# Optimization experiments

Measured on AMD Instinct MI355X. Metric: run time of the kernel, lower is better.

Reference implementation:

```python
import jax, jax.numpy as jnp
import numpy as np

B, N, D = 8, 2048, 768
K, H, G = 256, 12, 4
DH = D // H          # 64
EPS = 1e-12


def grouped_pointwise(x, w):
    """Grouped Conv1d with kernel_size=1, no bias.
    x: (b, n, d); w: (g, out_per_g, in_per_g) [torch weight (d, d/g, 1) reshaped].
    """
    b, n, d = x.shape
    g = w.shape[0]
    xg = x.reshape(b, n, g, d // g)
    return jnp.einsum('bngi,goi->bngo', xg, w).reshape(b, n, d)


def setup_inputs() -> dict:
    key = jax.random.key(0)
    ks = jax.random.split(key, 8)
    std_conv = 1.0 / np.sqrt(D // G)   # torch conv default ~ U(-sqrt(1/fan_in), ...)
    std_pk = 1.0 / np.sqrt(K)          # init_ uses last dim of (seq_len, k_dim)
    std_lin = 1.0 / np.sqrt(D)
    return {
        'input_embedding': jax.random.normal(ks[0], (B, N, D), jnp.float32),
        'wq': jax.random.uniform(ks[1], (G, D // G, D // G), jnp.float32, -std_conv, std_conv),
        'wk': jax.random.uniform(ks[2], (G, D // G, D // G), jnp.float32, -std_conv, std_conv),
        'project_k': jax.random.uniform(ks[3], (N, K), jnp.float32, -std_pk, std_pk),
        'w_out': jax.random.uniform(ks[4], (D, D), jnp.float32, -std_lin, std_lin),
        'b_out': jax.random.uniform(ks[5], (D,), jnp.float32, -std_lin, std_lin),
        'gamma': jnp.ones((D,), jnp.float32),
        'beta': jnp.zeros((D,), jnp.float32),
    }


def reference(input_embedding, wq, wk, project_k, w_out, b_out, gamma, beta):
    x = input_embedding                       # (b, n, d)
    b, n, d = x.shape

    queries = grouped_pointwise(x, wq)        # (b, n, d)
    k_raw = grouped_pointwise(x, wk)          # (b, n, d)  (key conv)
    k_proj = jnp.einsum('bnd,nk->bkd', k_raw, project_k)   # (b, K, d)

    # Faithful replication of: keys.permute(0,2,1).view(b, K, h, dh)
    # (memory-reinterpreting reshape of the (b, d, K) layout)
    keys = jnp.transpose(k_proj, (0, 2, 1)).reshape(b, K, H, DH)
    keys = jnp.transpose(keys, (0, 2, 1, 3))                # (b, h, K, dh)

    # values also come from the key conv (self.value unused in source forward)
    values = k_proj.reshape(b, K, H, DH).transpose(0, 2, 1, 3)   # (b, h, K, dh)
    q = queries.reshape(b, n, H, DH).transpose(0, 2, 1, 3)       # (b, h, n, dh)

    dots = jnp.einsum('bhnd,bhkd->bhnk', q, keys) / np.sqrt(DH)
    attn = jax.nn.softmax(dots, axis=-1)      # dropout = identity (eval)
    ctx = jnp.einsum('bhnk,bhkd->bhnd', attn, values)
    ctx = ctx.transpose(0, 2, 1, 3).reshape(b, n, d)

    out = ctx @ w_out.T + b_out               # nn.Linear
    y = x + out                               # residual
    mu = jnp.mean(y, axis=-1, keepdims=True)
    var = jnp.mean((y - mu) ** 2, axis=-1, keepdims=True)
    return (y - mu) / jnp.sqrt(var + EPS) * gamma + beta
```

## Files before the change

### kernel.cpp

```cpp
#include <hip/hip_runtime.h>
#include <hip/hip_bf16.h>

typedef short short8 __attribute__((ext_vector_type(8)));
typedef short short4v __attribute__((ext_vector_type(4)));
typedef int i32x4 __attribute__((ext_vector_type(4)));
typedef float f32x4 __attribute__((ext_vector_type(4)));

#define MFMA(a, b, c) __builtin_amdgcn_mfma_f32_16x16x32_bf16((a), (b), (c), 0, 0, 0)

__device__ __forceinline__ short f2bf(float f) {
  unsigned u = __builtin_bit_cast(unsigned, f);
  unsigned r = u + 0x7FFFu + ((u >> 16) & 1u);
  return (short)(r >> 16);
}

__device__ __forceinline__ float bf2f(short s) {
  unsigned u = ((unsigned)(unsigned short)s) << 16;
  return __builtin_bit_cast(float, u);
}

__device__ __forceinline__ short8 cvt8(float4 a, float4 b) {
  short8 t;
  t[0] = f2bf(a.x); t[1] = f2bf(a.y); t[2] = f2bf(a.z); t[3] = f2bf(a.w);
  t[4] = f2bf(b.x); t[5] = f2bf(b.y); t[6] = f2bf(b.z); t[7] = f2bf(b.w);
  return t;
}

__global__ __launch_bounds__(256) void k_prep_xt(
    const float* __restrict__ wq, const float* __restrict__ wk,
    const float* __restrict__ wout, const float* __restrict__ pk,
    short* __restrict__ wqb, short* __restrict__ wkb,
    short* __restrict__ woutb, short* __restrict__ pkT,
    const float* __restrict__ x, short* __restrict__ xbT)
{
  __shared__ short Ls[64][78];
  const int bid = blockIdx.x, tid = threadIdx.x;
  if (bid < 2304) {
    int idx = bid * 256 + tid;
    if (idx < 147456) { wqb[idx] = f2bf(wq[idx]); wkb[idx] = f2bf(wk[idx]); }
    if (idx < 589824) { woutb[idx] = f2bf(wout[idx]); }
    if (idx < 524288) {
      int n = idx >> 8, k = idx & 255;
      pkT[(size_t)k * 2048 + n] = f2bf(pk[idx]);
    }
    return;
  }
  const int bid2 = bid - 2304;
  const int e0 = (bid2 % 12) * 64;
  const int n0 = ((bid2 / 12) % 32) * 64;
  const int b  = bid2 / 384;
  const int r = tid >> 2, ci = (tid & 3) * 16;
  const float* src = x + ((size_t)b * 2048 + n0 + r) * 768 + e0 + ci;
#pragma unroll
  for (int ii = 0; ii < 4; ii++) {
    float4 v = *(const float4*)(src + ii * 4);
    short4v s; s[0] = f2bf(v.x); s[1] = f2bf(v.y); s[2] = f2bf(v.z); s[3] = f2bf(v.w);
    *(short4v*)&Ls[r][ci + ii * 4] = s;
  }
  __syncthreads();
  const int ep = tid >> 2, no = (tid & 3) * 16;
  short8 o0, o1;
#pragma unroll
  for (int u = 0; u < 8; u++) o0[u] = Ls[no + u][ep];
#pragma unroll
  for (int u = 0; u < 8; u++) o1[u] = Ls[no + 8 + u][ep];
  short* dst = xbT + ((size_t)b * 768 + e0 + ep) * 2048 + n0 + no;
  *(short8*)dst = o0;
  *(short8*)(dst + 8) = o1;
}

__global__ __launch_bounds__(256, 2) void k_conv(
    const float* __restrict__ x, const short* __restrict__ wqb,
    short* __restrict__ qo)
{
  __shared__ __align__(16) short Xs[64][40];
  const int tid = threadIdx.x, lane = tid & 63, w = tid >> 6;
  const int g = blockIdx.y;
  const int m0 = blockIdx.x * 64;
  const int wr = (w >> 1) * 32, wcol = (w & 1) * 96;
  const int lrow = lane & 15, lk8 = (lane >> 4) * 8;

  f32x4 acc[2][6];
#pragma unroll
  for (int mi = 0; mi < 2; mi++)
#pragma unroll
    for (int cf = 0; cf < 6; cf++) acc[mi][cf] = (f32x4)0.f;

  const int xr = tid >> 2;
  const int xc = (tid & 3) * 8;
  const float* xsrc = x + (size_t)(m0 + xr) * 768 + g * 192 + xc;

  for (int k0 = 0; k0 < 192; k0 += 32) {
    __syncthreads();
    {
      float4 v0 = *(const float4*)(xsrc + k0);
      float4 v1 = *(const float4*)(xsrc + k0 + 4);
      *(short8*)&Xs[xr][xc] = cvt8(v0, v1);
    }
    __syncthreads();
    short8 a0 = *(const short8*)&Xs[wr + lrow][lk8];
    short8 a1 = *(const short8*)&Xs[wr + 16 + lrow][lk8];
#pragma unroll
    for (int cf = 0; cf < 6; cf++) {
      short8 bb = *(const short8*)(wqb + ((size_t)g * 192 + wcol + cf * 16 + lrow) * 192 + k0 + lk8);
      acc[0][cf] = MFMA(a0, bb, acc[0][cf]);
      acc[1][cf] = MFMA(a1, bb, acc[1][cf]);
    }
  }
#pragma unroll
  for (int mi = 0; mi < 2; mi++)
#pragma unroll
    for (int cf = 0; cf < 6; cf++)
#pragma unroll
      for (int j = 0; j < 4; j++) {
        int m = m0 + wr + mi * 16 + (lane >> 4) * 4 + j;
        qo[(size_t)m * 768 + g * 192 + wcol + cf * 16 + lrow] = f2bf(acc[mi][cf][j]);
      }
}

__global__ __launch_bounds__(512, 4) void k_xproj(
    const short* __restrict__ pkT, const short* __restrict__ xbT,
    float* __restrict__ xproj)
{
  __shared__ __align__(16) short A2[2][64][72];
  __shared__ __align__(16) short B2[2][64][72];
  const int tid = threadIdx.x, lane = tid & 63, w = tid >> 6;
  const int f = blockIdx.x;
  const int xcd = f & 7, rem = f >> 3;
  const int k2t4 = rem & 3, eb8 = rem >> 2;
  const int e_b = eb8 * 8 + xcd;
  const int k2t = k2t4 * 64;
  const int et = (e_b % 12) * 64, b = e_b / 12;
  const int lrow = lane & 15, g4 = lane >> 4, lk8 = g4 * 8;
  const int wa = (w & 3) * 16, wb = (w >> 2) * 32;

  const int r = tid >> 3, c8 = tid & 7;
  const short* aSrc = pkT + (size_t)(k2t + r) * 2048 + c8 * 8;
  const short* bSrc = xbT + ((size_t)b * 768 + et + r) * 2048 + c8 * 8;

  {
    short8 gA = *(const short8*)aSrc;
    short8 gB = *(const short8*)bSrc;
    *(short8*)&A2[0][r][c8 * 8] = gA;
    *(short8*)&B2[0][r][c8 * 8] = gB;
  }
  __syncthreads();

  f32x4 acc[2];
  acc[0] = (f32x4)0.f; acc[1] = (f32x4)0.f;

  short8 gA, gB;
#pragma unroll 2
  for (int t = 0; t < 32; ++t) {
    const int cur = t & 1;
    if (t < 31) {
      gA = *(const short8*)(aSrc + (t + 1) * 64);
      gB = *(const short8*)(bSrc + (t + 1) * 64);
    }
    short8 af0 = *(const short8*)&A2[cur][wa + lrow][lk8];
    short8 af1 = *(const short8*)&A2[cur][wa + lrow][32 + lk8];
    short8 bf00 = *(const short8*)&B2[cur][wb + lrow][lk8];
    short8 bf01 = *(const short8*)&B2[cur][wb + lrow][32 + lk8];
    short8 bf10 = *(const short8*)&B2[cur][wb + 16 + lrow][lk8];
    short8 bf11 = *(const short8*)&B2[cur][wb + 16 + lrow][32 + lk8];
    acc[0] = MFMA(af0, bf00, acc[0]);
    acc[0] = MFMA(af1, bf01, acc[0]);
    acc[1] = MFMA(af0, bf10, acc[1]);
    acc[1] = MFMA(af1, bf11, acc[1]);
    if (t < 31) {
      *(short8*)&A2[cur ^ 1][r][c8 * 8] = gA;
      *(short8*)&B2[cur ^ 1][r][c8 * 8] = gB;
    }
    __syncthreads();
  }

  float* dst = xproj + ((size_t)b * 256 + k2t + wa) * 768 + et + wb;
#pragma unroll
  for (int cf = 0; cf < 2; cf++)
#pragma unroll
    for (int j = 0; j < 4; j++)
      dst[(size_t)(g4 * 4 + j) * 768 + cf * 16 + lrow] = acc[cf][j];
}

__global__ __launch_bounds__(256) void k_kconv(
    float* xpio, const short* __restrict__ wkb)
{
  const int tid = threadIdx.x, lane = tid & 63, w = tid >> 6;
  const int rt = blockIdx.x * 64, g = blockIdx.y, b = blockIdx.z;
  const int wr = (w >> 1) * 32, wcol = (w & 1) * 96;
  const int lrow = lane & 15, g4 = lane >> 4, lk8 = (lane >> 4) * 8;

  f32x4 acc[2][6];
#pragma unroll
  for (int mi = 0; mi < 2; mi++)
#pragma unroll
    for (int cf = 0; cf < 6; cf++) acc[mi][cf] = (f32x4)0.f;

#pragma unroll
  for (int s = 0; s < 6; s++) {
    int k0 = s * 32;
    short8 af[2];
#pragma unroll
    for (int mi = 0; mi < 2; mi++) {
      const float* ap = xpio + ((size_t)b * 256 + rt + wr + mi * 16 + lrow) * 768
                        + g * 192 + k0 + lk8;
      float4 f0 = *(const float4*)ap;
      float4 f1 = *(const float4*)(ap + 4);
      af[mi] = cvt8(f0, f1);
    }
#pragma unroll
    for (int cf = 0; cf < 6; cf++) {
      short8 bb = *(const short8*)(wkb + ((size_t)g * 192 + wcol + cf * 16 + lrow) * 192 + k0 + lk8);
      acc[0][cf] = MFMA(af[0], bb, acc[0][cf]);
      acc[1][cf] = MFMA(af[1], bb, acc[1][cf]);
    }
  }
  __syncthreads();
#pragma unroll
  for (int mi = 0; mi < 2; mi++)
#pragma unroll
    for (int cf = 0; cf < 6; cf++)
#pragma unroll
      for (int j = 0; j < 4; j++) {
        int k2 = rt + wr + mi * 16 + g4 * 4 + j;
        xpio[((size_t)b * 256 + k2) * 768 + g * 192 + wcol + cf * 16 + lrow] =
            acc[mi][cf][j];
      }
}

__global__ __launch_bounds__(256) void k_gather(
    const float* __restrict__ kp, short* __restrict__ Kb, short* __restrict__ Vb)
{
  const int h = blockIdx.x, b = blockIdx.y;
  const int bh = b * 12 + h;
  const int tid = threadIdx.x;
  const float* kpb = kp + (size_t)b * 196608;
  {
    const int kb4 = (h & 3) * 64, doff = h >> 2;
    const int dh = tid & 63, kq = tid >> 6;
    const float* row = kpb + (size_t)(kb4 + dh) * 768 + doff;
    short* dst = Kb + (size_t)bh * 18432 + dh;
#pragma unroll 8
    for (int i = 0; i < 64; i++) {
      int k2 = kq * 64 + i;
      dst[(size_t)k2 * 72] = f2bf(row[3 * k2]);
    }
  }
  {
    short* dst = Vb + (size_t)bh * 16384;
#pragma unroll
    for (int i = 0; i < 8; i++) {
      int oct = tid + 256 * i;
      int k2h = oct >> 6, dh = oct & 63;
      short8 v;
#pragma unroll
      for (int u = 0; u < 8; u++)
        v[u] = f2bf(kpb[(size_t)(k2h * 8 + u) * 768 + h * 64 + dh]);
      *(short8*)&dst[oct * 8] = v;
    }
  }
}

__global__ __launch_bounds__(512, 4) void k_attn(
    const short* __restrict__ qws, const short* __restrict__ Kb,
    const short* __restrict__ Vb, short* __restrict__ ctx)
{
  __shared__ __align__(16) short Kls[18432];
  __shared__ __align__(16) short Vls[16384];
  const int tid = threadIdx.x, lane = tid & 63, w = tid >> 6;
  const int n0 = blockIdx.x * 128;
  const int h = blockIdx.y, b = blockIdx.z;
  const int bh = b * 12 + h;

  {
    const short8* gk = (const short8*)(Kb + (size_t)bh * 18432);
    short8* lk = (short8*)Kls;
#pragma unroll
    for (int i = 0; i < 4; i++) lk[tid + 512 * i] = gk[tid + 512 * i];
    if (tid < 256) lk[tid + 2048] = gk[tid + 2048];
    const short8* gv = (const short8*)(Vb + (size_t)bh * 16384);
    short8* lv = (short8*)Vls;
#pragma unroll
    for (int i = 0; i < 4; i++) lv[tid + 512 * i] = gv[tid + 512 * i];
  }
  const int lrow = lane & 15, g = lane >> 4, lk8 = g * 8;
  const int nrow = n0 + w * 16;
  const short* qp = qws + ((size_t)b * 2048 + nrow + lrow) * 768 + h * 64;
  short8 bq0 = *(const short8*)(qp + lk8);
  short8 bq1 = *(const short8*)(qp + 32 + lk8);
  __syncthreads();

  f32x4 s[16];
#pragma unroll
  for (int fc = 0; fc < 16; fc++) s[fc] = (f32x4)0.f;
  __builtin_amdgcn_s_setprio(1);
#pragma unroll
  for (int fc = 0; fc < 16; fc++) {
    short8 ak0 = *(const short8*)&Kls[(fc * 16 + lrow) * 72 + lk8];
    short8 ak1 = *(const short8*)&Kls[(fc * 16 + lrow) * 72 + 32 + lk8];
    s[fc] = MFMA(ak0, bq0, s[fc]);
    s[fc] = MFMA(ak1, bq1, s[fc]);
  }
  __builtin_amdgcn_s_setprio(0);

  float mx = -3.0e38f;
#pragma unroll
  for (int fc = 0; fc < 16; fc++)
#pragma unroll
    for (int j = 0; j < 4; j++) mx = fmaxf(mx, s[fc][j]);
  mx = fmaxf(mx, __shfl_xor(mx, 16));
  mx = fmaxf(mx, __shfl_xor(mx, 32));
  float sum = 0.f;
#pragma unroll
  for (int fc = 0; fc < 16; fc++)
#pragma unroll
    for (int j = 0; j < 4; j++) {
      float e = __expf(0.125f * (s[fc][j] - mx));
      s[fc][j] = e; sum += e;
    }
  sum += __shfl_xor(sum, 16);
  sum += __shfl_xor(sum, 32);
  float inv = 1.f / sum;

  unsigned pku[16][2];
#pragma unroll
  for (int fc = 0; fc < 16; fc++) {
    pku[fc][0] = (unsigned)(unsigned short)f2bf(s[fc][0] * inv)
               | ((unsigned)(unsigned short)f2bf(s[fc][1] * inv) << 16);
    pku[fc][1] = (unsigned)(unsigned short)f2bf(s[fc][2] * inv)
               | ((unsigned)(unsigned short)f2bf(s[fc][3] * inv) << 16);
  }

  f32x4 o[4];
#pragma unroll
  for (int fd = 0; fd < 4; fd++) o[fd] = (f32x4)0.f;
  const int L0 = ((lane & 16) << 1) + lrow;
  const int L1 = L0 + 16;
  const bool hi = (lane >= 32);
  __builtin_amdgcn_s_setprio(1);
#pragma unroll
  for (int t = 0; t < 8; t++) {
    unsigned a0 = (unsigned)__shfl((int)pku[2 * t][0], L0);
    unsigned a1 = (unsigned)__shfl((int)pku[2 * t][1], L0);
    unsigned a2 = (unsigned)__shfl((int)pku[2 * t][0], L1);
    unsigned a3 = (unsigned)__shfl((int)pku[2 * t][1], L1);
    unsigned c0 = (unsigned)__shfl((int)pku[2 * t + 1][0], L0);
    unsigned c1 = (unsigned)__shfl((int)pku[2 * t + 1][1], L0);
    unsigned c2 = (unsigned)__shfl((int)pku[2 * t + 1][0], L1);
    unsigned c3 = (unsigned)__shfl((int)pku[2 * t + 1][1], L1);
    i32x4 bi = { (int)(hi ? c0 : a0), (int)(hi ? c1 : a1),
                 (int)(hi ? c2 : a2), (int)(hi ? c3 : a3) };
    short8 bfrag = __builtin_bit_cast(short8, bi);
#pragma unroll
    for (int fd = 0; fd < 4; fd++) {
      short8 av = *(const short8*)&Vls[((t * 4 + g) * 64 + fd * 16 + lrow) * 8];
      o[fd] = MFMA(av, bfrag, o[fd]);
    }
  }
  __builtin_amdgcn_s_setprio(0);
#pragma unroll
  for (int fd = 0; fd < 4; fd++) {
    short4v st;
#pragma unroll
    for (int j = 0; j < 4; j++) st[j] = f2bf(o[fd][j]);
    *(short4v*)&ctx[((size_t)b * 2048 + n0 + w * 16 + lrow) * 768
                    + h * 64 + fd * 16 + 4 * g] = st;
  }
}

__global__ __launch_bounds__(512, 4) void k_gemm_y(
    const short* __restrict__ ctx, const short* __restrict__ woutb,
    const float* __restrict__ bout, const float* __restrict__ x,
    short* __restrict__ ybf)
{
  __shared__ __align__(16) short As[2][128][40];
  __shared__ __align__(16) short Bs[2][128][40];
  const int tid = threadIdx.x, lane = tid & 63, w = tid >> 6;
  const int f = blockIdx.x;
  const int xcd = f & 7, rem = f >> 3;
  const int mi_l = rem / 6, ni = rem % 6;
  const int m0 = (xcd * 16 + mi_l) * 128;
  const int n0 = ni * 128;
  const int lrow = lane & 15, g4 = lane >> 4, lk8 = g4 * 8;
  const int wr2 = (w >> 2) * 64, wc4 = (w & 3) * 32;

  const int r = tid >> 2, c8 = (tid & 3) * 8;
  const short* aSrc = ctx + (size_t)(m0 + r) * 768 + c8;
  const short* bSrc = woutb + (size_t)(n0 + r) * 768 + c8;

  {
    short8 gA = *(const short8*)aSrc;
    short8 gB = *(const short8*)bSrc;
    *(short8*)&As[0][r][c8] = gA;
    *(short8*)&Bs[0][r][c8] = gB;
  }
  __syncthreads();

  f32x4 acc[4][2];
#pragma unroll
  for (int rf = 0; rf < 4; rf++)
#pragma unroll
    for (int cf = 0; cf < 2; cf++) acc[rf][cf] = (f32x4)0.f;

  short8 gA, gB;
#pragma unroll 2
  for (int t = 0; t < 24; ++t) {
    const int cur = t & 1;
    if (t < 23) {
      gA = *(const short8*)(aSrc + (t + 1) * 32);
      gB = *(const short8*)(bSrc + (t + 1) * 32);
    }
    short8 af[4], bf[2];
#pragma unroll
    for (int rf = 0; rf < 4; rf++)
      af[rf] = *(const short8*)&As[cur][wr2 + rf * 16 + lrow][lk8];
#pragma unroll
    for (int cf = 0; cf < 2; cf++)
      bf[cf] = *(const short8*)&Bs[cur][wc4 + cf * 16 + lrow][lk8];
#pragma unroll
    for (int cf = 0; cf < 2; cf++)
#pragma unroll
      for (int rf = 0; rf < 4; rf++)
        acc[rf][cf] = MFMA(af[rf], bf[cf], acc[rf][cf]);
    if (t < 23) {
      *(short8*)&As[cur ^ 1][r][c8] = gA;
      *(short8*)&Bs[cur ^ 1][r][c8] = gB;
    }
    __syncthreads();
  }

  float cB[2];
#pragma unroll
  for (int cf = 0; cf < 2; cf++) cB[cf] = bout[n0 + wc4 + cf * 16 + lrow];
#pragma unroll
  for (int rf = 0; rf < 4; rf++)
#pragma unroll
    for (int j = 0; j < 4; j++) {
      int row = m0 + wr2 + rf * 16 + g4 * 4 + j;
      const float* xr = x + (size_t)row * 768 + n0 + wc4;
      short* yr = ybf + (size_t)row * 768 + n0 + wc4;
#pragma unroll
      for (int cf = 0; cf < 2; cf++)
        yr[cf * 16 + lrow] = f2bf(acc[rf][cf][j] + cB[cf] + xr[cf * 16 + lrow]);
    }
}

__global__ __launch_bounds__(256) void k_ln(
    const short* __restrict__ ybf, const float* __restrict__ gamma,
    const float* __restrict__ beta, float* __restrict__ out)
{
  const int tid = threadIdx.x, lane = tid & 63, w = tid >> 6;
  const int half = lane >> 5, l5 = lane & 31;
  const int row = blockIdx.x * 8 + w * 2 + half;
  const short* yr = ybf + (size_t)row * 768;

  float v[24];
  float s1 = 0.f, s2 = 0.f;
#pragma unroll
  for (int j = 0; j < 3; j++) {
    short8 p = *(const short8*)(yr + (l5 + 32 * j) * 8);
#pragma unroll
    for (int u = 0; u < 8; u++) {
      float fv = bf2f(p[u]);
      v[j * 8 + u] = fv;
      s1 += fv; s2 += fv * fv;
    }
  }
  s1 += __shfl_xor(s1, 1, 32);  s2 += __shfl_xor(s2, 1, 32);
  s1 += __shfl_xor(s1, 2, 32);  s2 += __shfl_xor(s2, 2, 32);
  s1 += __shfl_xor(s1, 4, 32);  s2 += __shfl_xor(s2, 4, 32);
  s1 += __shfl_xor(s1, 8, 32);  s2 += __shfl_xor(s2, 8, 32);
  s1 += __shfl_xor(s1, 16, 32); s2 += __shfl_xor(s2, 16, 32);
  float mean = s1 * (1.f / 768.f);
  float var = s2 * (1.f / 768.f) - mean * mean;
  float rstd = rsqrtf(var + 1e-12f);

  float* orow = out + (size_t)row * 768;
#pragma unroll
  for (int j = 0; j < 3; j++) {
    int c0 = (l5 + 32 * j) * 8;
    float4 o0, o1;
    o0.x = (v[j*8+0] - mean) * rstd * gamma[c0+0] + beta[c0+0];
    o0.y = (v[j*8+1] - mean) * rstd * gamma[c0+1] + beta[c0+1];
    o0.z = (v[j*8+2] - mean) * rstd * gamma[c0+2] + beta[c0+2];
    o0.w = (v[j*8+3] - mean) * rstd * gamma[c0+3] + beta[c0+3];
    o1.x = (v[j*8+4] - mean) * rstd * gamma[c0+4] + beta[c0+4];
    o1.y = (v[j*8+5] - mean) * rstd * gamma[c0+5] + beta[c0+5];
    o1.z = (v[j*8+6] - mean) * rstd * gamma[c0+6] + beta[c0+6];
    o1.w = (v[j*8+7] - mean) * rstd * gamma[c0+7] + beta[c0+7];
    *(float4*)(orow + c0) = o0;
    *(float4*)(orow + c0 + 4) = o1;
  }
}

extern "C" void kernel_launch(void* const* d_in, const int* in_sizes, int n_in,
                              void* d_out, int out_size, void* d_ws, size_t ws_size,
                              hipStream_t stream)
{
  const float* x     = (const float*)d_in[0];
  const float* wq    = (const float*)d_in[1];
  const float* wk    = (const float*)d_in[2];
  const float* pk    = (const float*)d_in[3];
  const float* wout  = (const float*)d_in[4];
  const float* bout  = (const float*)d_in[5];
  const float* gamma = (const float*)d_in[6];
  const float* beta  = (const float*)d_in[7];
  float* out = (float*)d_out;

  char* ws = (char*)d_ws;
  short* qbf   = (short*)(ws + 0);
  short* xbT   = (short*)(ws + 25165824);
  float* kpbuf = (float*)(ws + 50331648);
  short* wqb   = (short*)(ws + 56623104);
  short* wkb   = (short*)(ws + 56918016);
  short* woutb = (short*)(ws + 57212928);
  short* pkT   = (short*)(ws + 58392576);
  if (ws_size < 59441152) return;
  short* ctx = (short*)xbT;
  short* ybf = qbf;

  short* Kb = (short*)d_out;
  short* Vb = Kb + 96 * 18432;

  k_prep_xt<<<2304 + 3072, 256, 0, stream>>>(wq, wk, wout, pk, wqb, wkb, woutb,
                                             pkT, x, xbT);
  k_conv<<<dim3(256, 4), 256, 0, stream>>>(x, wqb, qbf);
  k_xproj<<<384, 512, 0, stream>>>(pkT, xbT, kpbuf);
  k_kconv<<<dim3(4, 4, 8), 256, 0, stream>>>(kpbuf, wkb);
  k_gather<<<dim3(12, 8), 256, 0, stream>>>(kpbuf, Kb, Vb);
  k_attn<<<dim3(16, 12, 8), 512, 0, stream>>>(qbf, Kb, Vb, ctx);
  k_gemm_y<<<768, 512, 0, stream>>>(ctx, woutb, bout, x, ybf);
  k_ln<<<2048, 256, 0, stream>>>(ybf, gamma, beta, out);
}
```

Measured before the change: 172.7 us.

## Fuse x transpose into conv and fuse output GEMM with LayerNorm

The bf16 transpose of x now happens inside k_conv: it stages the whole 64x192 input tile in swizzled LDS, computes the grouped conv from it, and writes the transposed copy from the same tile. This removes a separate pass that read x again. The output GEMM now has each 64-row block compute all 768 columns and apply bias, residual and LayerNorm in registers, which drops the bf16 y round trip and the k_ln launch. In exchange the fused GEMM launches only 256 blocks with a 64x768 tile, 24 accumulators per thread and a large LDS buffer for B. That lowers occupancy and parallelism and reloads W_out for every block.

```diff
diff --git a/kernel.cpp b/kernel.cpp
--- a/kernel.cpp
+++ b/kernel.cpp
@@ -26,59 +26,45 @@
   return t;
 }
 
-__global__ __launch_bounds__(256) void k_prep_xt(
+__global__ __launch_bounds__(256) void k_prep(
     const float* __restrict__ wq, const float* __restrict__ wk,
     const float* __restrict__ wout, const float* __restrict__ pk,
     short* __restrict__ wqb, short* __restrict__ wkb,
-    short* __restrict__ woutb, short* __restrict__ pkT,
-    const float* __restrict__ x, short* __restrict__ xbT)
-{
-  __shared__ short Ls[64][78];
-  const int bid = blockIdx.x, tid = threadIdx.x;
-  if (bid < 2304) {
-    int idx = bid * 256 + tid;
-    if (idx < 147456) { wqb[idx] = f2bf(wq[idx]); wkb[idx] = f2bf(wk[idx]); }
-    if (idx < 589824) { woutb[idx] = f2bf(wout[idx]); }
-    if (idx < 524288) {
-      int n = idx >> 8, k = idx & 255;
-      pkT[(size_t)k * 2048 + n] = f2bf(pk[idx]);
-    }
-    return;
-  }
-  const int bid2 = bid - 2304;
-  const int e0 = (bid2 % 12) * 64;
-  const int n0 = ((bid2 / 12) % 32) * 64;
-  const int b  = bid2 / 384;
-  const int r = tid >> 2, ci = (tid & 3) * 16;
-  const float* src = x + ((size_t)b * 2048 + n0 + r) * 768 + e0 + ci;
-#pragma unroll
-  for (int ii = 0; ii < 4; ii++) {
-    float4 v = *(const float4*)(src + ii * 4);
-    short4v s; s[0] = f2bf(v.x); s[1] = f2bf(v.y); s[2] = f2bf(v.z); s[3] = f2bf(v.w);
-    *(short4v*)&Ls[r][ci + ii * 4] = s;
-  }
-  __syncthreads();
-  const int ep = tid >> 2, no = (tid & 3) * 16;
-  short8 o0, o1;
-#pragma unroll
-  for (int u = 0; u < 8; u++) o0[u] = Ls[no + u][ep];
-#pragma unroll
-  for (int u = 0; u < 8; u++) o1[u] = Ls[no + 8 + u][ep];
-  short* dst = xbT + ((size_t)b * 768 + e0 + ep) * 2048 + n0 + no;
-  *(short8*)dst = o0;
-  *(short8*)(dst + 8) = o1;
+    short* __restrict__ woutb, short* __restrict__ pkT)
+{
+  int idx = blockIdx.x * 256 + threadIdx.x;
+  if (idx < 147456) { wqb[idx] = f2bf(wq[idx]); wkb[idx] = f2bf(wk[idx]); }
+  if (idx < 589824) { woutb[idx] = f2bf(wout[idx]); }
+  if (idx < 524288) {
+    int n = idx >> 8, k = idx & 255;
+    pkT[(size_t)k * 2048 + n] = f2bf(pk[idx]);
+  }
 }
 
 __global__ __launch_bounds__(256, 2) void k_conv(
     const float* __restrict__ x, const short* __restrict__ wqb,
-    short* __restrict__ qo)
-{
-  __shared__ __align__(16) short Xs[64][40];
+    short* __restrict__ qo, short* __restrict__ xbT)
+{
+  __shared__ __align__(16) short Xs[64 * 192];
   const int tid = threadIdx.x, lane = tid & 63, w = tid >> 6;
   const int g = blockIdx.y;
   const int m0 = blockIdx.x * 64;
   const int wr = (w >> 1) * 32, wcol = (w & 1) * 96;
-  const int lrow = lane & 15, lk8 = (lane >> 4) * 8;
+  const int lrow = lane & 15, g4 = lane >> 4, lk8 = g4 * 8;
+
+  {
+    const int r = tid >> 2, cb = (tid & 3) * 48;
+    const int sw = (r ^ (r >> 3)) & 7;
+    const float* src = x + (size_t)(m0 + r) * 768 + g * 192 + cb;
+#pragma unroll
+    for (int i = 0; i < 6; i++) {
+      float4 v0 = *(const float4*)(src + i * 8);
+      float4 v1 = *(const float4*)(src + i * 8 + 4);
+      int o = (cb >> 3) + i;
+      *(short8*)&Xs[r * 192 + ((o ^ sw) << 3)] = cvt8(v0, v1);
+    }
+  }
+  __syncthreads();
 
   f32x4 acc[2][6];
 #pragma unroll
@@ -86,20 +72,16 @@
 #pragma unroll
     for (int cf = 0; cf < 6; cf++) acc[mi][cf] = (f32x4)0.f;
 
-  const int xr = tid >> 2;
-  const int xc = (tid & 3) * 8;
-  const float* xsrc = x + (size_t)(m0 + xr) * 768 + g * 192 + xc;
-
-  for (int k0 = 0; k0 < 192; k0 += 32) {
-    __syncthreads();
-    {
-      float4 v0 = *(const float4*)(xsrc + k0);
-      float4 v1 = *(const float4*)(xsrc + k0 + 4);
-      *(short8*)&Xs[xr][xc] = cvt8(v0, v1);
-    }
-    __syncthreads();
-    short8 a0 = *(const short8*)&Xs[wr + lrow][lk8];
-    short8 a1 = *(const short8*)&Xs[wr + 16 + lrow][lk8];
+  const int row0 = wr + lrow, row1 = wr + 16 + lrow;
+  const int sw0 = (row0 ^ (row0 >> 3)) & 7;
+  const int sw1 = (row1 ^ (row1 >> 3)) & 7;
+
+#pragma unroll
+  for (int s = 0; s < 6; s++) {
+    const int k0 = s * 32;
+    const int ob = (k0 >> 3) + g4;
+    short8 a0 = *(const short8*)&Xs[row0 * 192 + ((ob ^ sw0) << 3)];
+    short8 a1 = *(const short8*)&Xs[row1 * 192 + ((ob ^ sw1) << 3)];
 #pragma unroll
     for (int cf = 0; cf < 6; cf++) {
       short8 bb = *(const short8*)(wqb + ((size_t)g * 192 + wcol + cf * 16 + lrow) * 192 + k0 + lk8);
@@ -107,15 +89,33 @@
       acc[1][cf] = MFMA(a1, bb, acc[1][cf]);
     }
   }
+
 #pragma unroll
   for (int mi = 0; mi < 2; mi++)
 #pragma unroll
     for (int cf = 0; cf < 6; cf++)
 #pragma unroll
       for (int j = 0; j < 4; j++) {
-        int m = m0 + wr + mi * 16 + (lane >> 4) * 4 + j;
+        int m = m0 + wr + mi * 16 + g4 * 4 + j;
         qo[(size_t)m * 768 + g * 192 + wcol + cf * 16 + lrow] = f2bf(acc[mi][cf][j]);
       }
+
+  {
+    const int b = m0 >> 11, n0 = m0 & 2047;
+    const int el = tid >> 3, oct = tid & 7;
+#pragma unroll
+    for (int ec = 0; ec < 6; ec++) {
+      const int c = ec * 32 + el;
+      const int o = c >> 3, ci = c & 7;
+      short8 v;
+#pragma unroll
+      for (int u = 0; u < 8; u++) {
+        const int n = oct * 8 + u;
+        v[u] = Xs[n * 192 + (((o ^ (u ^ oct)) << 3)) + ci];
+      }
+      *(short8*)(xbT + ((size_t)b * 768 + g * 192 + c) * 2048 + n0 + oct * 8) = v;
+    }
+  }
 }
 
 __global__ __launch_bounds__(512, 4) void k_xproj(
@@ -368,128 +368,113 @@
   }
 }
 
-__global__ __launch_bounds__(512, 4) void k_gemm_y(
+__global__ __launch_bounds__(512, 2) void k_gemm_yln(
     const short* __restrict__ ctx, const short* __restrict__ woutb,
     const float* __restrict__ bout, const float* __restrict__ x,
-    short* __restrict__ ybf)
-{
-  __shared__ __align__(16) short As[2][128][40];
-  __shared__ __align__(16) short Bs[2][128][40];
+    const float* __restrict__ gamma, const float* __restrict__ beta,
+    float* __restrict__ out)
+{
+  __shared__ __align__(16) short As[64][40];
+  __shared__ __align__(16) short Bs[768][40];
   const int tid = threadIdx.x, lane = tid & 63, w = tid >> 6;
-  const int f = blockIdx.x;
-  const int xcd = f & 7, rem = f >> 3;
-  const int mi_l = rem / 6, ni = rem % 6;
-  const int m0 = (xcd * 16 + mi_l) * 128;
-  const int n0 = ni * 128;
+  const int m0 = blockIdx.x * 64;
   const int lrow = lane & 15, g4 = lane >> 4, lk8 = g4 * 8;
-  const int wr2 = (w >> 2) * 64, wc4 = (w & 3) * 32;
-
-  const int r = tid >> 2, c8 = (tid & 3) * 8;
-  const short* aSrc = ctx + (size_t)(m0 + r) * 768 + c8;
-  const short* bSrc = woutb + (size_t)(n0 + r) * 768 + c8;
-
-  {
-    short8 gA = *(const short8*)aSrc;
-    short8 gB = *(const short8*)bSrc;
-    *(short8*)&As[0][r][c8] = gA;
-    *(short8*)&Bs[0][r][c8] = gB;
+  const int wr = w >> 1;
+  const int wc = w & 1;
+  const int colbase = wc * 384;
+
+  const int rb = tid >> 2, c8 = (tid & 3) * 8;
+  const short* aSrc = ctx + (size_t)(m0 + rb) * 768 + c8;
+  const short* bSrc = woutb + (size_t)rb * 768 + c8;
+
+  {
+    if (tid < 256) *(short8*)&As[rb][c8] = *(const short8*)aSrc;
+#pragma unroll
+    for (int i = 0; i < 6; i++)
+      *(short8*)&Bs[rb + 128 * i][c8] = *(const short8*)(bSrc + (size_t)i * 98304);
   }
   __syncthreads();
 
-  f32x4 acc[4][2];
-#pragma unroll
-  for (int rf = 0; rf < 4; rf++)
-#pragma unroll
-    for (int cf = 0; cf < 2; cf++) acc[rf][cf] = (f32x4)0.f;
-
-  short8 gA, gB;
+  f32x4 acc[24];
+#pragma unroll
+  for (int cf = 0; cf < 24; cf++) acc[cf] = (f32x4)0.f;
+
+  short8 pA;
+  short8 pB[6];
 #pragma unroll 2
   for (int t = 0; t < 24; ++t) {
-    const int cur = t & 1;
     if (t < 23) {
-      gA = *(const short8*)(aSrc + (t + 1) * 32);
-      gB = *(const short8*)(bSrc + (t + 1) * 32);
-    }
-    short8 af[4], bf[2];
-#pragma unroll
-    for (int rf = 0; rf < 4; rf++)
-      af[rf] = *(const short8*)&As[cur][wr2 + rf * 16 + lrow][lk8];
-#pragma unroll
-    for (int cf = 0; cf < 2; cf++)
-      bf[cf] = *(const short8*)&Bs[cur][wc4 + cf * 16 + lrow][lk8];
-#pragma unroll
-    for (int cf = 0; cf < 2; cf++)
-#pragma unroll
-      for (int rf = 0; rf < 4; rf++)
-        acc[rf][cf] = MFMA(af[rf], bf[cf], acc[rf][cf]);
+      if (tid < 256) pA = *(const short8*)(aSrc + (t + 1) * 32);
+#pragma unroll
+      for (int i = 0; i < 6; i++)
+        pB[i] = *(const short8*)(bSrc + (size_t)i * 98304 + (t + 1) * 32);
+    }
+    short8 af = *(const short8*)&As[wr * 16 + lrow][lk8];
+#pragma unroll
+    for (int cf = 0; cf < 24; cf++) {
+      short8 bf = *(const short8*)&Bs[colbase + cf * 16 + lrow][lk8];
+      acc[cf] = MFMA(af, bf, acc[cf]);
+    }
+    __syncthreads();
     if (t < 23) {
-      *(short8*)&As[cur ^ 1][r][c8] = gA;
-      *(short8*)&Bs[cur ^ 1][r][c8] = gB;
+      if (tid < 256) *(short8*)&As[rb][c8] = pA;
+#pragma unroll
+      for (int i = 0; i < 6; i++)
+        *(short8*)&Bs[rb + 128 * i][c8] = pB[i];
     }
     __syncthreads();
   }
 
-  float cB[2];
-#pragma unroll
-  for (int cf = 0; cf < 2; cf++) cB[cf] = bout[n0 + wc4 + cf * 16 + lrow];
-#pragma unroll
-  for (int rf = 0; rf < 4; rf++)
+  float s1[4] = {0.f, 0.f, 0.f, 0.f}, s2[4] = {0.f, 0.f, 0.f, 0.f};
+#pragma unroll
+  for (int cf = 0; cf < 24; cf++) {
+    const int col = colbase + cf * 16 + lrow;
+    float bb = bout[col];
 #pragma unroll
     for (int j = 0; j < 4; j++) {
-      int row = m0 + wr2 + rf * 16 + g4 * 4 + j;
-      const float* xr = x + (size_t)row * 768 + n0 + wc4;
-      short* yr = ybf + (size_t)row * 768 + n0 + wc4;
-#pragma unroll
-      for (int cf = 0; cf < 2; cf++)
-        yr[cf * 16 + lrow] = f2bf(acc[rf][cf][j] + cB[cf] + xr[cf * 16 + lrow]);
-    }
-}
-
-__global__ __launch_bounds__(256) void k_ln(
-    const short* __restrict__ ybf, const float* __restrict__ gamma,
-    const float* __restrict__ beta, float* __restrict__ out)
-{
-  const int tid = threadIdx.x, lane = tid & 63, w = tid >> 6;
-  const int half = lane >> 5, l5 = lane & 31;
-  const int row = blockIdx.x * 8 + w * 2 + half;
-  const short* yr = ybf + (size_t)row * 768;
-
-  float v[24];
-  float s1 = 0.f, s2 = 0.f;
-#pragma unroll
-  for (int j = 0; j < 3; j++) {
-    short8 p = *(const short8*)(yr + (l5 + 32 * j) * 8);
-#pragma unroll
-    for (int u = 0; u < 8; u++) {
-      float fv = bf2f(p[u]);
-      v[j * 8 + u] = fv;
-      s1 += fv; s2 += fv * fv;
-    }
-  }
-  s1 += __shfl_xor(s1, 1, 32);  s2 += __shfl_xor(s2, 1, 32);
-  s1 += __shfl_xor(s1, 2, 32);  s2 += __shfl_xor(s2, 2, 32);
-  s1 += __shfl_xor(s1, 4, 32);  s2 += __shfl_xor(s2, 4, 32);
-  s1 += __shfl_xor(s1, 8, 32);  s2 += __shfl_xor(s2, 8, 32);
-  s1 += __shfl_xor(s1, 16, 32); s2 += __shfl_xor(s2, 16, 32);
-  float mean = s1 * (1.f / 768.f);
-  float var = s2 * (1.f / 768.f) - mean * mean;
-  float rstd = rsqrtf(var + 1e-12f);
-
-  float* orow = out + (size_t)row * 768;
-#pragma unroll
-  for (int j = 0; j < 3; j++) {
-    int c0 = (l5 + 32 * j) * 8;
-    float4 o0, o1;
-    o0.x = (v[j*8+0] - mean) * rstd * gamma[c0+0] + beta[c0+0];
-    o0.y = (v[j*8+1] - mean) * rstd * gamma[c0+1] + beta[c0+1];
-    o0.z = (v[j*8+2] - mean) * rstd * gamma[c0+2] + beta[c0+2];
-    o0.w = (v[j*8+3] - mean) * rstd * gamma[c0+3] + beta[c0+3];
-    o1.x = (v[j*8+4] - mean) * rstd * gamma[c0+4] + beta[c0+4];
-    o1.y = (v[j*8+5] - mean) * rstd * gamma[c0+5] + beta[c0+5];
-    o1.z = (v[j*8+6] - mean) * rstd * gamma[c0+6] + beta[c0+6];
-    o1.w = (v[j*8+7] - mean) * rstd * gamma[c0+7] + beta[c0+7];
-    *(float4*)(orow + c0) = o0;
-    *(float4*)(orow + c0 + 4) = o1;
+      const int row = m0 + wr * 16 + g4 * 4 + j;
+      float yv = acc[cf][j] + bb + x[(size_t)row * 768 + col];
+      acc[cf][j] = yv;
+      s1[j] += yv; s2[j] += yv * yv;
+    }
+  }
+#pragma unroll
+  for (int m = 1; m < 16; m <<= 1) {
+#pragma unroll
+    for (int j = 0; j < 4; j++) {
+      s1[j] += __shfl_xor(s1[j], m);
+      s2[j] += __shfl_xor(s2[j], m);
+    }
+  }
+  float2* red = (float2*)&As[0][0];
+  if (lrow == 0) {
+#pragma unroll
+    for (int j = 0; j < 4; j++) {
+      float2 t; t.x = s1[j]; t.y = s2[j];
+      red[wc * 64 + wr * 16 + g4 * 4 + j] = t;
+    }
+  }
+  __syncthreads();
+  float mean_[4], rstd_[4];
+#pragma unroll
+  for (int j = 0; j < 4; j++) {
+    const int rl = wr * 16 + g4 * 4 + j;
+    float2 p0 = red[rl], p1 = red[64 + rl];
+    float S1 = p0.x + p1.x, S2 = p0.y + p1.y;
+    float mu = S1 * (1.f / 768.f);
+    float var = S2 * (1.f / 768.f) - mu * mu;
+    mean_[j] = mu;
+    rstd_[j] = rsqrtf(var + 1e-12f);
+  }
+#pragma unroll
+  for (int cf = 0; cf < 24; cf++) {
+    const int col = colbase + cf * 16 + lrow;
+    float gm = gamma[col], bt = beta[col];
+#pragma unroll
+    for (int j = 0; j < 4; j++) {
+      const int row = m0 + wr * 16 + g4 * 4 + j;
+      out[(size_t)row * 768 + col] = (acc[cf][j] - mean_[j]) * rstd_[j] * gm + bt;
+    }
   }
 }
 
@@ -517,18 +502,15 @@
   short* pkT   = (short*)(ws + 58392576);
   if (ws_size < 59441152) return;
   short* ctx = (short*)xbT;
-  short* ybf = qbf;
 
   short* Kb = (short*)d_out;
   short* Vb = Kb + 96 * 18432;
 
-  k_prep_xt<<<2304 + 3072, 256, 0, stream>>>(wq, wk, wout, pk, wqb, wkb, woutb,
-                                             pkT, x, xbT);
-  k_conv<<<dim3(256, 4), 256, 0, stream>>>(x, wqb, qbf);
+  k_prep<<<2304, 256, 0, stream>>>(wq, wk, wout, pk, wqb, wkb, woutb, pkT);
+  k_conv<<<dim3(256, 4), 256, 0, stream>>>(x, wqb, qbf, xbT);
   k_xproj<<<384, 512, 0, stream>>>(pkT, xbT, kpbuf);
   k_kconv<<<dim3(4, 4, 8), 256, 0, stream>>>(kpbuf, wkb);
   k_gather<<<dim3(12, 8), 256, 0, stream>>>(kpbuf, Kb, Vb);
   k_attn<<<dim3(16, 12, 8), 512, 0, stream>>>(qbf, Kb, Vb, ctx);
-  k_gemm_y<<<768, 512, 0, stream>>>(ctx, woutb, bout, x, ybf);
-  k_ln<<<2048, 256, 0, stream>>>(ybf, gamma, beta, out);
-}
+  k_gemm_yln<<<256, 512, 0, stream>>>(ctx, woutb, bout, x, gamma, beta, out);
+}
```

New measurement: 169.9 us. Within noise of the previous version (-1.6%).

## Fuse bf16 transpose of x into Q conv kernel using swizzled LDS tile

Applied to the files above, without the earlier changes.

The separate pass that read x, converted it to bf16 and wrote the transposed xbT is removed from the prep kernel. The Q grouped-conv kernel now loads its full 64x192 x tile into LDS once, using an XOR swizzle, and reuses that tile both for the MFMA A operands and to write the transposed bf16 copy. This avoids reading x from global memory a second time and drops the per-k-step barriers. The cost is a larger LDS footprint per block, which may lower occupancy, plus strided LDS reads for the transpose.

```diff
diff --git a/kernel.cpp b/kernel.cpp
--- a/kernel.cpp
+++ b/kernel.cpp
@@ -26,59 +26,45 @@
   return t;
 }
 
-__global__ __launch_bounds__(256) void k_prep_xt(
+__global__ __launch_bounds__(256) void k_prep(
     const float* __restrict__ wq, const float* __restrict__ wk,
     const float* __restrict__ wout, const float* __restrict__ pk,
     short* __restrict__ wqb, short* __restrict__ wkb,
-    short* __restrict__ woutb, short* __restrict__ pkT,
-    const float* __restrict__ x, short* __restrict__ xbT)
-{
-  __shared__ short Ls[64][78];
-  const int bid = blockIdx.x, tid = threadIdx.x;
-  if (bid < 2304) {
-    int idx = bid * 256 + tid;
-    if (idx < 147456) { wqb[idx] = f2bf(wq[idx]); wkb[idx] = f2bf(wk[idx]); }
-    if (idx < 589824) { woutb[idx] = f2bf(wout[idx]); }
-    if (idx < 524288) {
-      int n = idx >> 8, k = idx & 255;
-      pkT[(size_t)k * 2048 + n] = f2bf(pk[idx]);
-    }
-    return;
-  }
-  const int bid2 = bid - 2304;
-  const int e0 = (bid2 % 12) * 64;
-  const int n0 = ((bid2 / 12) % 32) * 64;
-  const int b  = bid2 / 384;
-  const int r = tid >> 2, ci = (tid & 3) * 16;
-  const float* src = x + ((size_t)b * 2048 + n0 + r) * 768 + e0 + ci;
-#pragma unroll
-  for (int ii = 0; ii < 4; ii++) {
-    float4 v = *(const float4*)(src + ii * 4);
-    short4v s; s[0] = f2bf(v.x); s[1] = f2bf(v.y); s[2] = f2bf(v.z); s[3] = f2bf(v.w);
-    *(short4v*)&Ls[r][ci + ii * 4] = s;
-  }
-  __syncthreads();
-  const int ep = tid >> 2, no = (tid & 3) * 16;
-  short8 o0, o1;
-#pragma unroll
-  for (int u = 0; u < 8; u++) o0[u] = Ls[no + u][ep];
-#pragma unroll
-  for (int u = 0; u < 8; u++) o1[u] = Ls[no + 8 + u][ep];
-  short* dst = xbT + ((size_t)b * 768 + e0 + ep) * 2048 + n0 + no;
-  *(short8*)dst = o0;
-  *(short8*)(dst + 8) = o1;
+    short* __restrict__ woutb, short* __restrict__ pkT)
+{
+  int idx = blockIdx.x * 256 + threadIdx.x;
+  if (idx < 147456) { wqb[idx] = f2bf(wq[idx]); wkb[idx] = f2bf(wk[idx]); }
+  if (idx < 589824) { woutb[idx] = f2bf(wout[idx]); }
+  if (idx < 524288) {
+    int n = idx >> 8, k = idx & 255;
+    pkT[(size_t)k * 2048 + n] = f2bf(pk[idx]);
+  }
 }
 
 __global__ __launch_bounds__(256, 2) void k_conv(
     const float* __restrict__ x, const short* __restrict__ wqb,
-    short* __restrict__ qo)
-{
-  __shared__ __align__(16) short Xs[64][40];
+    short* __restrict__ qo, short* __restrict__ xbT)
+{
+  __shared__ __align__(16) short Xs[64 * 192];
   const int tid = threadIdx.x, lane = tid & 63, w = tid >> 6;
   const int g = blockIdx.y;
   const int m0 = blockIdx.x * 64;
   const int wr = (w >> 1) * 32, wcol = (w & 1) * 96;
-  const int lrow = lane & 15, lk8 = (lane >> 4) * 8;
+  const int lrow = lane & 15, g4 = lane >> 4, lk8 = g4 * 8;
+
+  {
+    const int r = tid >> 2, cb = (tid & 3) * 48;
+    const int sw = (r ^ (r >> 3)) & 7;
+    const float* src = x + (size_t)(m0 + r) * 768 + g * 192 + cb;
+#pragma unroll
+    for (int i = 0; i < 6; i++) {
+      float4 v0 = *(const float4*)(src + i * 8);
+      float4 v1 = *(const float4*)(src + i * 8 + 4);
+      int o = (cb >> 3) + i;
+      *(short8*)&Xs[r * 192 + ((o ^ sw) << 3)] = cvt8(v0, v1);
+    }
+  }
+  __syncthreads();
 
   f32x4 acc[2][6];
 #pragma unroll
@@ -86,20 +72,16 @@
 #pragma unroll
     for (int cf = 0; cf < 6; cf++) acc[mi][cf] = (f32x4)0.f;
 
-  const int xr = tid >> 2;
-  const int xc = (tid & 3) * 8;
-  const float* xsrc = x + (size_t)(m0 + xr) * 768 + g * 192 + xc;
-
-  for (int k0 = 0; k0 < 192; k0 += 32) {
-    __syncthreads();
-    {
-      float4 v0 = *(const float4*)(xsrc + k0);
-      float4 v1 = *(const float4*)(xsrc + k0 + 4);
-      *(short8*)&Xs[xr][xc] = cvt8(v0, v1);
-    }
-    __syncthreads();
-    short8 a0 = *(const short8*)&Xs[wr + lrow][lk8];
-    short8 a1 = *(const short8*)&Xs[wr + 16 + lrow][lk8];
+  const int row0 = wr + lrow, row1 = wr + 16 + lrow;
+  const int sw0 = (row0 ^ (row0 >> 3)) & 7;
+  const int sw1 = (row1 ^ (row1 >> 3)) & 7;
+
+#pragma unroll
+  for (int s = 0; s < 6; s++) {
+    const int k0 = s * 32;
+    const int ob = (k0 >> 3) + g4;
+    short8 a0 = *(const short8*)&Xs[row0 * 192 + ((ob ^ sw0) << 3)];
+    short8 a1 = *(const short8*)&Xs[row1 * 192 + ((ob ^ sw1) << 3)];
 #pragma unroll
     for (int cf = 0; cf < 6; cf++) {
       short8 bb = *(const short8*)(wqb + ((size_t)g * 192 + wcol + cf * 16 + lrow) * 192 + k0 + lk8);
@@ -107,6 +89,7 @@
       acc[1][cf] = MFMA(a1, bb, acc[1][cf]);
     }
   }
+
 #pragma unroll
   for (int mi = 0; mi < 2; mi++)
 #pragma unroll
@@ -116,6 +99,23 @@
         int m = m0 + wr + mi * 16 + (lane >> 4) * 4 + j;
         qo[(size_t)m * 768 + g * 192 + wcol + cf * 16 + lrow] = f2bf(acc[mi][cf][j]);
       }
+
+  {
+    const int b = m0 >> 11, n0 = m0 & 2047;
+    const int el = tid >> 3, oct = tid & 7;
+#pragma unroll
+    for (int ec = 0; ec < 6; ec++) {
+      const int c = ec * 32 + el;
+      const int o = c >> 3, ci = c & 7;
+      short8 v;
+#pragma unroll
+      for (int u = 0; u < 8; u++) {
+        const int n = oct * 8 + u;
+        v[u] = Xs[n * 192 + (((o ^ (u ^ oct)) << 3)) + ci];
+      }
+      *(short8*)(xbT + ((size_t)b * 768 + g * 192 + c) * 2048 + n0 + oct * 8) = v;
+    }
+  }
 }
 
 __global__ __launch_bounds__(512, 4) void k_xproj(
@@ -522,9 +522,8 @@
   short* Kb = (short*)d_out;
   short* Vb = Kb + 96 * 18432;
 
-  k_prep_xt<<<2304 + 3072, 256, 0, stream>>>(wq, wk, wout, pk, wqb, wkb, woutb,
-                                             pkT, x, xbT);
-  k_conv<<<dim3(256, 4), 256, 0, stream>>>(x, wqb, qbf);
+  k_prep<<<2304, 256, 0, stream>>>(wq, wk, wout, pk, wqb, wkb, woutb, pkT);
+  k_conv<<<dim3(256, 4), 256, 0, stream>>>(x, wqb, qbf, xbT);
   k_xproj<<<384, 512, 0, stream>>>(pkT, xbT, kpbuf);
   k_kconv<<<dim3(4, 4, 8), 256, 0, stream>>>(kpbuf, wkb);
   k_gather<<<dim3(12, 8), 256, 0, stream>>>(kpbuf, Kb, Vb);
```

New measurement: 166.6 us. 1.04x faster.
